# Kernel tuning notes

Measured on AMD Instinct MI355X. Metric: run time of the kernel, lower is better.

## Reference

```python
import jax, jax.numpy as jnp
import numpy as np
from jax import lax

B, H, T = 4096, 300, 64  # batch, hidden (=z_dim=WORD_DIM), SENTENCE_LEN


def setup_inputs() -> dict:
    key = jax.random.key(0)
    ks = jax.random.split(key, 9)
    s = 0.05  # small init so tanh/sigmoid gates stay well-conditioned
    return {
        "z": jax.random.uniform(ks[0], (B, H), dtype=jnp.float32),
        "W_ih0": jax.random.normal(ks[1], (4 * H, H), dtype=jnp.float32) * s,
        "W_hh0": jax.random.normal(ks[2], (4 * H, H), dtype=jnp.float32) * s,
        "b_ih0": jax.random.normal(ks[3], (4 * H,), dtype=jnp.float32) * s,
        "b_hh0": jax.random.normal(ks[4], (4 * H,), dtype=jnp.float32) * s,
        "W_ih1": jax.random.normal(ks[5], (4 * H, H), dtype=jnp.float32) * s,
        "W_hh1": jax.random.normal(ks[6], (4 * H, H), dtype=jnp.float32) * s,
        "b_ih1": jax.random.normal(ks[7], (4 * H,), dtype=jnp.float32) * s,
        "b_hh1": jax.random.normal(ks[8], (4 * H,), dtype=jnp.float32) * s,
        "sentence_len": T,
    }


def _lstm_cell(x, h, c, W_ih, W_hh, b_ih, b_hh):
    # PyTorch gate order: input, forget, cell(g), output
    gates = x @ W_ih.T + h @ W_hh.T + (b_ih + b_hh)  # [B, 4H]
    i, f, g, o = jnp.split(gates, 4, axis=-1)
    i = jax.nn.sigmoid(i)
    f = jax.nn.sigmoid(f)
    g = jnp.tanh(g)
    o = jax.nn.sigmoid(o)
    c_new = f * c + i * g
    h_new = o * jnp.tanh(c_new)
    return h_new, c_new


def reference(z, W_ih0, W_hh0, b_ih0, b_hh0, W_ih1, W_hh1, b_ih1, b_hh1, sentence_len):
    b, hdim = z.shape
    h0 = jnp.zeros((b, hdim), z.dtype)
    c0 = jnp.zeros((b, hdim), z.dtype)

    def step(carry, _):
        x, h0_, c0_, h1_, c1_ = carry
        h0n, c0n = _lstm_cell(x, h0_, c0_, W_ih0, W_hh0, b_ih0, b_hh0)
        h1n, c1n = _lstm_cell(h0n, h1_, c1_, W_ih1, W_hh1, b_ih1, b_hh1)
        # top-layer output is fed back as next-step input
        return (h1n, h0n, c0n, h1n, c1n), h1n

    _, ys = lax.scan(step, (z, h0, c0, h0, c0), None, length=sentence_len)
    # ys: [T, B, H] -> [B, 1, T, H] (matches stack(dim=1).unsqueeze(1))
    return jnp.transpose(ys, (1, 0, 2))[:, None, :, :]
```

## Files before the change

### kernel.cpp

```cpp
#include <hip/hip_runtime.h>

#define BATCH    4096
#define HDIM     300
#define GDIM     1200
#define TSTEPS   64
#define NKT      19
#define NTILES   75
#define ASTRIDE  616
#define HSTRIDE  304
#define OUTSTRIDE (TSTEPS*HDIM)
#define ROWS     16
#define NWAVES   8
#define PFK      16

typedef _Float16 half8  __attribute__((ext_vector_type(8)));
typedef float    floatx4 __attribute__((ext_vector_type(4)));

#define WP_LAYER_ELEMS ((size_t)NTILES * NKT * 512)

__global__ void pack_weights(const float* __restrict__ Wih0, const float* __restrict__ Whh0,
                             const float* __restrict__ Wih1, const float* __restrict__ Whh1,
                             _Float16* __restrict__ wp) {
    int idx = blockIdx.x * 256 + threadIdx.x;
    const int total = 2 * NTILES * NKT * 64;
    if (idx >= total) return;
    int lane  = idx & 63;
    int rest  = idx >> 6;
    int kt    = rest % NKT;
    int rest2 = rest / NKT;
    int tile  = rest2 % NTILES;
    int l     = rest2 / NTILES;
    const float* Wih = l ? Wih1 : Wih0;
    const float* Whh = l ? Whh1 : Whh0;
    int n    = tile * 16 + (lane & 15);
    int hcol = n >> 2, gate = n & 3;
    int jrow = gate * 300 + hcol;
    int k0   = kt * 32 + (lane >> 4) * 8;
    half8 v8;
#pragma unroll
    for (int j = 0; j < 8; ++j) {
        int k = k0 + j;
        float v = 0.f;
        if (k < 300)      v = Wih[jrow * 300 + k];
        else if (k < 600) v = Whh[jrow * 300 + (k - 300)];
        v8[j] = (_Float16)v;
    }
    *(half8*)(wp + (size_t)idx * 8) = v8;
}

__global__ void pack_bias(const float* __restrict__ bih0, const float* __restrict__ bhh0,
                          const float* __restrict__ bih1, const float* __restrict__ bhh1,
                          float* __restrict__ bp) {
    int idx = blockIdx.x * 256 + threadIdx.x;
    if (idx >= 2 * GDIM) return;
    int l = idx / GDIM, n = idx % GDIM;
    int hcol = n >> 2, gate = n & 3;
    int j = gate * 300 + hcol;
    bp[idx] = l ? (bih1[j] + bhh1[j]) : (bih0[j] + bhh0[j]);
}

__device__ __forceinline__ float sigmoid_f(float x) {
    return 1.f / (1.f + __expf(-x));
}
__device__ __forceinline__ float tanh_f(float x) {
    x = fminf(fmaxf(x, -15.f), 15.f);
    float e = __expf(2.f * x);
    return (e - 1.f) / (e + 1.f);
}

__global__ __launch_bounds__(512, 2)
void lstm_kernel(const float* __restrict__ z, const _Float16* __restrict__ wp,
                 const float* __restrict__ bp, float* __restrict__ out) {
    __shared__ _Float16 A0[ROWS * ASTRIDE];
    __shared__ _Float16 A1[ROWS * ASTRIDE];
    __shared__ float    bias_lds[2 * GDIM];
    __shared__ __align__(16) float scratch[NWAVES * 16 * 20];
    __shared__ float    Hst[2][ROWS * HSTRIDE];
    __shared__ float    Cst[2][ROWS * HSTRIDE];

    const int tid  = threadIdx.x;
    const int wave = tid >> 6;
    const int lane = tid & 63;
    const int row0 = blockIdx.x * ROWS;

    for (int i = tid; i < ROWS * ASTRIDE; i += 512) {
        int r = i / ASTRIDE, c = i - r * ASTRIDE;
        A0[i] = (_Float16)((c < HDIM) ? z[(size_t)(row0 + r) * HDIM + c] : 0.f);
        A1[i] = (_Float16)0.f;
    }
    for (int i = tid; i < 2 * GDIM; i += 512) bias_lds[i] = bp[i];
    for (int i = tid; i < ROWS * HSTRIDE; i += 512) { Cst[0][i] = 0.f; Cst[1][i] = 0.f; }
    __syncthreads();

    const int m    = lane & 15;
    const int quad = lane >> 4;
    float* myscr = scratch + wave * (16 * 20);
    const int NT = (82 - wave) / 8;
    const size_t tstep = (size_t)8 * NKT * 512;

    for (int t = 0; t < TSTEPS; ++t) {
#pragma unroll
        for (int l = 0; l < 2; ++l) {
            const _Float16* Asrc = l ? A1 : A0;
            _Float16*       Adst = l ? A0 : A1;
            const _Float16* wpl  = wp + (size_t)l * WP_LAYER_ELEMS;
            const float*    bl   = bias_lds + l * GDIM;
            float* cst = Cst[l];
            float* hst = Hst[l];

            half8 areg[NKT];
            {
                const _Float16* arow = Asrc + m * ASTRIDE + quad * 8;
#pragma unroll
                for (int kt = 0; kt < NKT; ++kt) areg[kt] = *(const half8*)(arow + kt * 32);
            }

            const _Float16* wt = wpl + (size_t)wave * (NKT * 512) + lane * 8;

            auto process = [&](int i, half8 (&bc)[PFK], half8 (&bn)[PFK]) {
                const _Float16* wcur = wt + (size_t)i * tstep;
                half8 bt[NKT - PFK];
#pragma unroll
                for (int kt = PFK; kt < NKT; ++kt)
                    bt[kt - PFK] = *(const half8*)(wcur + kt * 512);
                if (i + 1 < NT) {
                    const _Float16* wnext = wcur + tstep;
#pragma unroll
                    for (int kt = 0; kt < PFK; ++kt)
                        bn[kt] = *(const half8*)(wnext + kt * 512);
                }
                floatx4 acc = {0.f, 0.f, 0.f, 0.f};
#pragma unroll
                for (int kt = 0; kt < PFK; ++kt)
                    acc = __builtin_amdgcn_mfma_f32_16x16x32_f16(areg[kt], bc[kt], acc, 0, 0, 0);
#pragma unroll
                for (int kt = PFK; kt < NKT; ++kt)
                    acc = __builtin_amdgcn_mfma_f32_16x16x32_f16(areg[kt], bt[kt - PFK], acc, 0, 0, 0);

                const int tile = wave + 8 * i;
                float bn_ = bl[tile * 16 + m];
#pragma unroll
                for (int r = 0; r < 4; ++r)
                    myscr[(quad * 4 + r) * 20 + m] = acc[r] + bn_;
                __builtin_amdgcn_wave_barrier();
                floatx4 pg = *(const floatx4*)(myscr + m * 20 + quad * 4);
                __builtin_amdgcn_wave_barrier();
                float ig = sigmoid_f(pg.x);
                float fg = sigmoid_f(pg.y);
                float gg = tanh_f(pg.z);
                float og = sigmoid_f(pg.w);
                const int hcol = tile * 4 + quad;
                float c = fg * cst[m * HSTRIDE + hcol] + ig * gg;
                cst[m * HSTRIDE + hcol] = c;
                float h = og * tanh_f(c);
                hst[m * HSTRIDE + hcol] = h;
                Adst[m * ASTRIDE + hcol] = (_Float16)h;
            };

            half8 b0[PFK], b1[PFK];
#pragma unroll
            for (int kt = 0; kt < PFK; ++kt) b0[kt] = *(const half8*)(wt + kt * 512);

            int i = 0;
            while (true) {
                process(i, b0, b1); if (++i >= NT) break;
                process(i, b1, b0); if (++i >= NT) break;
            }

            __syncthreads();
            if (l == 0) {
                for (int idx = tid; idx < ROWS * HDIM; idx += 512) {
                    int r = idx / HDIM, c = idx - r * HDIM;
                    A0[r * ASTRIDE + 300 + c] = (_Float16)Hst[0][r * HSTRIDE + c];
                }
            } else {
                for (int idx = tid; idx < ROWS * HDIM; idx += 512) {
                    int r = idx / HDIM, c = idx - r * HDIM;
                    float h = Hst[1][r * HSTRIDE + c];
                    A1[r * ASTRIDE + 300 + c] = (_Float16)h;
                    __builtin_nontemporal_store(
                        h, out + (size_t)(row0 + r) * OUTSTRIDE + (size_t)t * HDIM + c);
                }
            }
        }
    }
}

extern "C" void kernel_launch(void* const* d_in, const int* in_sizes, int n_in,
                              void* d_out, int out_size, void* d_ws, size_t ws_size,
                              hipStream_t stream) {
    const float* z    = (const float*)d_in[0];
    const float* Wih0 = (const float*)d_in[1];
    const float* Whh0 = (const float*)d_in[2];
    const float* bih0 = (const float*)d_in[3];
    const float* bhh0 = (const float*)d_in[4];
    const float* Wih1 = (const float*)d_in[5];
    const float* Whh1 = (const float*)d_in[6];
    const float* bih1 = (const float*)d_in[7];
    const float* bhh1 = (const float*)d_in[8];
    float* out = (float*)d_out;

    _Float16* wp  = (_Float16*)d_ws;
    float*    bpf = (float*)((char*)d_ws + 2 * WP_LAYER_ELEMS * sizeof(_Float16));

    {
        int total = 2 * NTILES * NKT * 64;
        pack_weights<<<(total + 255) / 256, 256, 0, stream>>>(Wih0, Whh0, Wih1, Whh1, wp);
    }
    pack_bias<<<(2 * GDIM + 255) / 256, 256, 0, stream>>>(bih0, bhh0, bih1, bhh1, bpf);

    lstm_kernel<<<BATCH / ROWS, 512, 0, stream>>>(z, wp, bpf, out);
}
```

Measured before the change: 2.328 ms.

## Process 32 rows per block, reusing weight loads across two MFMA row tiles

Doubles the batch rows per block to 32 so each global weight fragment feeds two MFMA accumulators, halving weight traffic per row and halving the grid size. The input registers are read before a barrier, which lets new h values be written straight back into the A buffers. That removes the separate Hst staging and copy pass. Layer-1 cell state moves into registers, tile order is rotated per block to spread L2 access, and the activations use the fast reciprocal without clamping. Costs: the old weight prefetch pipeline is dropped, LDS and register pressure rise (which may reduce occupancy), and output stores become scattered scalar writes.

```diff
diff --git a/kernel.cpp b/kernel.cpp
--- a/kernel.cpp
+++ b/kernel.cpp
@@ -7,11 +7,10 @@
 #define NKT      19
 #define NTILES   75
 #define ASTRIDE  616
-#define HSTRIDE  304
+#define CSTRIDE  305
 #define OUTSTRIDE (TSTEPS*HDIM)
-#define ROWS     16
+#define ROWS     32
 #define NWAVES   8
-#define PFK      16
 
 typedef _Float16 half8  __attribute__((ext_vector_type(8)));
 typedef float    floatx4 __attribute__((ext_vector_type(4)));
@@ -60,23 +59,21 @@
 }
 
 __device__ __forceinline__ float sigmoid_f(float x) {
-    return 1.f / (1.f + __expf(-x));
+    return __builtin_amdgcn_rcpf(1.f + __expf(-x));
 }
 __device__ __forceinline__ float tanh_f(float x) {
-    x = fminf(fmaxf(x, -15.f), 15.f);
     float e = __expf(2.f * x);
-    return (e - 1.f) / (e + 1.f);
+    return 1.f - 2.f * __builtin_amdgcn_rcpf(e + 1.f);
 }
 
 __global__ __launch_bounds__(512, 2)
 void lstm_kernel(const float* __restrict__ z, const _Float16* __restrict__ wp,
                  const float* __restrict__ bp, float* __restrict__ out) {
-    __shared__ _Float16 A0[ROWS * ASTRIDE];
-    __shared__ _Float16 A1[ROWS * ASTRIDE];
-    __shared__ float    bias_lds[2 * GDIM];
+    __shared__ __align__(16) _Float16 A0[ROWS * ASTRIDE];
+    __shared__ __align__(16) _Float16 A1[ROWS * ASTRIDE];
+    __shared__ float bias_lds[2 * GDIM];
     __shared__ __align__(16) float scratch[NWAVES * 16 * 20];
-    __shared__ float    Hst[2][ROWS * HSTRIDE];
-    __shared__ float    Cst[2][ROWS * HSTRIDE];
+    __shared__ float Cst0[ROWS * CSTRIDE];
 
     const int tid  = threadIdx.x;
     const int wave = tid >> 6;
@@ -89,99 +86,123 @@
         A1[i] = (_Float16)0.f;
     }
     for (int i = tid; i < 2 * GDIM; i += 512) bias_lds[i] = bp[i];
-    for (int i = tid; i < ROWS * HSTRIDE; i += 512) { Cst[0][i] = 0.f; Cst[1][i] = 0.f; }
+    for (int i = tid; i < ROWS * CSTRIDE; i += 512) Cst0[i] = 0.f;
     __syncthreads();
 
     const int m    = lane & 15;
     const int quad = lane >> 4;
     float* myscr = scratch + wave * (16 * 20);
-    const int NT = (82 - wave) / 8;
+    const int NT  = (82 - wave) / 8;
+    const int rot = blockIdx.x % NT;
     const size_t tstep = (size_t)8 * NKT * 512;
 
+    float c1reg[10][2];
+#pragma unroll
+    for (int i = 0; i < 10; ++i) { c1reg[i][0] = 0.f; c1reg[i][1] = 0.f; }
+
     for (int t = 0; t < TSTEPS; ++t) {
-#pragma unroll
         for (int l = 0; l < 2; ++l) {
-            const _Float16* Asrc = l ? A1 : A0;
-            _Float16*       Adst = l ? A0 : A1;
-            const _Float16* wpl  = wp + (size_t)l * WP_LAYER_ELEMS;
-            const float*    bl   = bias_lds + l * GDIM;
-            float* cst = Cst[l];
-            float* hst = Hst[l];
-
-            half8 areg[NKT];
+            _Float16* Asrc = l ? A1 : A0;
+            _Float16* Adst = l ? A0 : A1;
+            const float* bl = bias_lds + l * GDIM;
+            const _Float16* wt = wp + (size_t)l * WP_LAYER_ELEMS
+                               + (size_t)wave * (NKT * 512) + lane * 8;
+
+            half8 a0[NKT], a1[NKT];
             {
-                const _Float16* arow = Asrc + m * ASTRIDE + quad * 8;
-#pragma unroll
-                for (int kt = 0; kt < NKT; ++kt) areg[kt] = *(const half8*)(arow + kt * 32);
+                const _Float16* ar0 = Asrc + m * ASTRIDE + quad * 8;
+                const _Float16* ar1 = ar0 + 16 * ASTRIDE;
+#pragma unroll
+                for (int kt = 0; kt < NKT; ++kt) {
+                    a0[kt] = *(const half8*)(ar0 + kt * 32);
+                    a1[kt] = *(const half8*)(ar1 + kt * 32);
+                }
             }
-
-            const _Float16* wt = wpl + (size_t)wave * (NKT * 512) + lane * 8;
-
-            auto process = [&](int i, half8 (&bc)[PFK], half8 (&bn)[PFK]) {
-                const _Float16* wcur = wt + (size_t)i * tstep;
-                half8 bt[NKT - PFK];
-#pragma unroll
-                for (int kt = PFK; kt < NKT; ++kt)
-                    bt[kt - PFK] = *(const half8*)(wcur + kt * 512);
-                if (i + 1 < NT) {
-                    const _Float16* wnext = wcur + tstep;
-#pragma unroll
-                    for (int kt = 0; kt < PFK; ++kt)
-                        bn[kt] = *(const half8*)(wnext + kt * 512);
-                }
-                floatx4 acc = {0.f, 0.f, 0.f, 0.f};
-#pragma unroll
-                for (int kt = 0; kt < PFK; ++kt)
-                    acc = __builtin_amdgcn_mfma_f32_16x16x32_f16(areg[kt], bc[kt], acc, 0, 0, 0);
-#pragma unroll
-                for (int kt = PFK; kt < NKT; ++kt)
-                    acc = __builtin_amdgcn_mfma_f32_16x16x32_f16(areg[kt], bt[kt - PFK], acc, 0, 0, 0);
-
-                const int tile = wave + 8 * i;
-                float bn_ = bl[tile * 16 + m];
-#pragma unroll
-                for (int r = 0; r < 4; ++r)
-                    myscr[(quad * 4 + r) * 20 + m] = acc[r] + bn_;
-                __builtin_amdgcn_wave_barrier();
-                floatx4 pg = *(const floatx4*)(myscr + m * 20 + quad * 4);
-                __builtin_amdgcn_wave_barrier();
-                float ig = sigmoid_f(pg.x);
-                float fg = sigmoid_f(pg.y);
-                float gg = tanh_f(pg.z);
-                float og = sigmoid_f(pg.w);
-                const int hcol = tile * 4 + quad;
-                float c = fg * cst[m * HSTRIDE + hcol] + ig * gg;
-                cst[m * HSTRIDE + hcol] = c;
-                float h = og * tanh_f(c);
-                hst[m * HSTRIDE + hcol] = h;
-                Adst[m * ASTRIDE + hcol] = (_Float16)h;
-            };
-
-            half8 b0[PFK], b1[PFK];
-#pragma unroll
-            for (int kt = 0; kt < PFK; ++kt) b0[kt] = *(const half8*)(wt + kt * 512);
-
-            int i = 0;
-            while (true) {
-                process(i, b0, b1); if (++i >= NT) break;
-                process(i, b1, b0); if (++i >= NT) break;
+            __syncthreads();
+
+#pragma unroll
+            for (int i = 0; i < 10; ++i) {
+                if (i >= NT) break;
+                int j = i + rot; if (j >= NT) j -= NT;
+                const int tile = wave + 8 * j;
+                const _Float16* wc = wt + (size_t)j * tstep;
+
+                floatx4 acc0 = {0.f, 0.f, 0.f, 0.f};
+                floatx4 acc1 = {0.f, 0.f, 0.f, 0.f};
+                half8 u[4], v[4];
+#pragma unroll
+                for (int k = 0; k < 4; ++k) u[k] = *(const half8*)(wc + k * 512);
+#pragma unroll
+                for (int k = 0; k < 4; ++k) v[k] = *(const half8*)(wc + (4 + k) * 512);
+#pragma unroll
+                for (int k = 0; k < 4; ++k) {
+                    acc0 = __builtin_amdgcn_mfma_f32_16x16x32_f16(a0[k], u[k], acc0, 0, 0, 0);
+                    acc1 = __builtin_amdgcn_mfma_f32_16x16x32_f16(a1[k], u[k], acc1, 0, 0, 0);
+                }
+#pragma unroll
+                for (int k = 0; k < 4; ++k) u[k] = *(const half8*)(wc + (8 + k) * 512);
+#pragma unroll
+                for (int k = 0; k < 4; ++k) {
+                    acc0 = __builtin_amdgcn_mfma_f32_16x16x32_f16(a0[4 + k], v[k], acc0, 0, 0, 0);
+                    acc1 = __builtin_amdgcn_mfma_f32_16x16x32_f16(a1[4 + k], v[k], acc1, 0, 0, 0);
+                }
+#pragma unroll
+                for (int k = 0; k < 4; ++k) v[k] = *(const half8*)(wc + (12 + k) * 512);
+#pragma unroll
+                for (int k = 0; k < 4; ++k) {
+                    acc0 = __builtin_amdgcn_mfma_f32_16x16x32_f16(a0[8 + k], u[k], acc0, 0, 0, 0);
+                    acc1 = __builtin_amdgcn_mfma_f32_16x16x32_f16(a1[8 + k], u[k], acc1, 0, 0, 0);
+                }
+#pragma unroll
+                for (int k = 0; k < 3; ++k) u[k] = *(const half8*)(wc + (16 + k) * 512);
+#pragma unroll
+                for (int k = 0; k < 4; ++k) {
+                    acc0 = __builtin_amdgcn_mfma_f32_16x16x32_f16(a0[12 + k], v[k], acc0, 0, 0, 0);
+                    acc1 = __builtin_amdgcn_mfma_f32_16x16x32_f16(a1[12 + k], v[k], acc1, 0, 0, 0);
+                }
+#pragma unroll
+                for (int k = 0; k < 3; ++k) {
+                    acc0 = __builtin_amdgcn_mfma_f32_16x16x32_f16(a0[16 + k], u[k], acc0, 0, 0, 0);
+                    acc1 = __builtin_amdgcn_mfma_f32_16x16x32_f16(a1[16 + k], u[k], acc1, 0, 0, 0);
+                }
+
+                const float bn_ = bl[tile * 16 + m];
+                const int hcol  = tile * 4 + quad;
+#pragma unroll
+                for (int r = 0; r < 4; ++r) myscr[(quad * 4 + r) * 20 + m] = acc0[r] + bn_;
+                __builtin_amdgcn_wave_barrier();
+                floatx4 pg0 = *(const floatx4*)(myscr + m * 20 + quad * 4);
+                __builtin_amdgcn_wave_barrier();
+#pragma unroll
+                for (int r = 0; r < 4; ++r) myscr[(quad * 4 + r) * 20 + m] = acc1[r] + bn_;
+                __builtin_amdgcn_wave_barrier();
+                floatx4 pg1 = *(const floatx4*)(myscr + m * 20 + quad * 4);
+                __builtin_amdgcn_wave_barrier();
+
+                {
+                    float ig = sigmoid_f(pg0.x), fg = sigmoid_f(pg0.y);
+                    float gg = tanh_f(pg0.z),    og = sigmoid_f(pg0.w);
+                    float cold = l ? c1reg[i][0] : Cst0[m * CSTRIDE + hcol];
+                    float cn = fg * cold + ig * gg;
+                    if (l) c1reg[i][0] = cn; else Cst0[m * CSTRIDE + hcol] = cn;
+                    float h = og * tanh_f(cn);
+                    Asrc[m * ASTRIDE + 300 + hcol] = (_Float16)h;
+                    Adst[m * ASTRIDE + hcol]       = (_Float16)h;
+                    if (l) out[(size_t)(row0 + m) * OUTSTRIDE + (size_t)t * HDIM + hcol] = h;
+                }
+                {
+                    float ig = sigmoid_f(pg1.x), fg = sigmoid_f(pg1.y);
+                    float gg = tanh_f(pg1.z),    og = sigmoid_f(pg1.w);
+                    float cold = l ? c1reg[i][1] : Cst0[(16 + m) * CSTRIDE + hcol];
+                    float cn = fg * cold + ig * gg;
+                    if (l) c1reg[i][1] = cn; else Cst0[(16 + m) * CSTRIDE + hcol] = cn;
+                    float h = og * tanh_f(cn);
+                    Asrc[(16 + m) * ASTRIDE + 300 + hcol] = (_Float16)h;
+                    Adst[(16 + m) * ASTRIDE + hcol]       = (_Float16)h;
+                    if (l) out[(size_t)(row0 + 16 + m) * OUTSTRIDE + (size_t)t * HDIM + hcol] = h;
+                }
             }
-
             __syncthreads();
-            if (l == 0) {
-                for (int idx = tid; idx < ROWS * HDIM; idx += 512) {
-                    int r = idx / HDIM, c = idx - r * HDIM;
-                    A0[r * ASTRIDE + 300 + c] = (_Float16)Hst[0][r * HSTRIDE + c];
-                }
-            } else {
-                for (int idx = tid; idx < ROWS * HDIM; idx += 512) {
-                    int r = idx / HDIM, c = idx - r * HDIM;
-                    float h = Hst[1][r * HSTRIDE + c];
-                    A1[r * ASTRIDE + 300 + c] = (_Float16)h;
-                    __builtin_nontemporal_store(
-                        h, out + (size_t)(row0 + r) * OUTSTRIDE + (size_t)t * HDIM + c);
-                }
-            }
         }
     }
 }
```

Measured after the change: 2.877 ms. +23.6%, slower.
